# Performance work log

Measured on AMD Instinct MI355X. Metric: run time of the kernel, lower is better.

## Reference

```python
import jax, jax.numpy as jnp
import numpy as np

NUM_HEADS = 16
D_MODEL = 1024
DEPTH = D_MODEL // NUM_HEADS
THRESHOLD = 0.1
BATCH = 2
SEQ = 2048


def setup_inputs() -> dict:
    key = jax.random.key(0)
    ks = jax.random.split(key, 9)
    w_scale = 1.0 / np.sqrt(D_MODEL)
    Q = jax.random.normal(ks[0], (BATCH, SEQ, D_MODEL), dtype=jnp.float32)
    T = jax.random.normal(ks[1], (BATCH, SEQ, D_MODEL), dtype=jnp.float32)
    V = jax.random.normal(ks[2], (BATCH, SEQ, D_MODEL), dtype=jnp.float32)
    Wq = jax.random.normal(ks[3], (NUM_HEADS, D_MODEL, DEPTH), dtype=jnp.float32) * w_scale
    Wk = jax.random.normal(ks[4], (NUM_HEADS, D_MODEL, DEPTH), dtype=jnp.float32) * w_scale
    Wv = jax.random.normal(ks[5], (NUM_HEADS, D_MODEL, DEPTH), dtype=jnp.float32) * w_scale
    Wo = jax.random.normal(ks[6], (D_MODEL, D_MODEL), dtype=jnp.float32) * w_scale
    bq = jnp.zeros((NUM_HEADS, DEPTH), dtype=jnp.float32)
    bk = jnp.zeros((NUM_HEADS, DEPTH), dtype=jnp.float32)
    bv = jnp.zeros((NUM_HEADS, DEPTH), dtype=jnp.float32)
    bo = jnp.zeros((D_MODEL,), dtype=jnp.float32)
    return {"Q": Q, "T": T, "V": V, "Wq": Wq, "bq": bq, "Wk": Wk, "bk": bk,
            "Wv": Wv, "bv": bv, "Wo": Wo, "bo": bo}


def reference(Q, T, V, Wq, bq, Wk, bk, Wv, bv, Wo, bo):
    # Per-head projections (stacked over heads): [B,S,D] x [H,D,E] -> [B,H,S,E]
    q = jnp.einsum('bsd,hde->bhse', Q, Wq) + bq[None, :, None, :]
    k = jnp.einsum('bsd,hde->bhse', T, Wk) + bk[None, :, None, :]
    v = jnp.einsum('bsd,hde->bhse', V, Wv) + bv[None, :, None, :]

    # Raw scores (NOT pre-scaled): [B,H,S,S]
    scores = jnp.einsum('bhqe,bhke->bhqk', q, k)
    # tf.where(A>thr, A, -2**32 * cast(A>thr)) -> failing entries become 0
    scores = jnp.where(scores > THRESHOLD, scores, jnp.zeros((), scores.dtype))
    # M = 1 - lower_band(ones): +1 on strictly upper-triangular entries
    seq = scores.shape[-1]
    upper = jnp.triu(jnp.ones((seq, seq), dtype=scores.dtype), k=1)
    scores = (scores + upper) / jnp.sqrt(jnp.asarray(DEPTH, scores.dtype))

    attn = jax.nn.softmax(scores, axis=-1)
    out = jnp.einsum('bhqk,bhke->bhqe', attn, v)  # [B,H,S,E]
    B, H, S, E = out.shape
    concat = out.transpose(0, 2, 1, 3).reshape(B, S, H * E)  # [B,S,D]
    return concat @ Wo + bo
```

## Files before the change

kernel.cpp:

```cpp
#include <hip/hip_runtime.h>
#include <stdint.h>


typedef __attribute__((ext_vector_type(8))) short bf16x8;
typedef __attribute__((ext_vector_type(4))) float f32x4;

#define DEVFN static __device__ __forceinline__

static constexpr int S_ = 2048;
static constexpr int H_ = 16;

DEVFN unsigned short f2bf(float x) {
  union { float f; uint32_t u; } v; v.f = x;
  const uint32_t r = v.u + 0x7fffu + ((v.u >> 16) & 1u);
  return (unsigned short)(r >> 16);
}

DEVFN f32x4 fzero() { f32x4 v = {0.f, 0.f, 0.f, 0.f}; return v; }

union U8 { uint32_t u[4]; bf16x8 v; };

DEVFN void gld_lds16(const void* g, void* lds) {
  __builtin_amdgcn_global_load_lds(
      (const __attribute__((address_space(1))) void*)g,
      (__attribute__((address_space(3))) void*)lds, 16, 0, 0);
}

__global__ void prep_weights(const float* __restrict__ Wq, const float* __restrict__ Wk,
                             const float* __restrict__ Wv, const float* __restrict__ Wo,
                             unsigned short* __restrict__ dstBase) {
  const int z = blockIdx.z;
  const float* src = (z == 0) ? Wq : (z == 1) ? Wk : (z == 2) ? Wv : Wo;
  unsigned short* dst = dstBase + (size_t)z * (1024u * 1024u);
  const int idx = blockIdx.x * 256 + threadIdx.x;
  const int c = idx & 1023;
  const int d0 = (idx >> 10) << 3;
  unsigned short hv[8];
#pragma unroll
  for (int t = 0; t < 8; ++t) {
    const int d = d0 + t;
    const float v = (z < 3) ? src[(size_t)((c >> 6) * 1024 + d) * 64 + (c & 63)]
                            : src[(size_t)d * 1024 + c];
    hv[t] = f2bf(v);
  }
  *(uint4*)(dst + (size_t)c * 1024 + d0) = *(const uint4*)hv;
}

__global__ __launch_bounds__(256, 3)
void proj_gemm(const float* __restrict__ Qm, const float* __restrict__ Tm,
               const float* __restrict__ Vm, const unsigned short* __restrict__ Wt,
               const float* __restrict__ bq, const float* __restrict__ bk,
               const float* __restrict__ bv, unsigned short* __restrict__ qb,
               unsigned short* __restrict__ kb, unsigned short* __restrict__ vtb) {
  __shared__ float Af[2][128 * 32];
  __shared__ unsigned short Bt[2][128 * 32];

  const int tid = threadIdx.x;
  const int lane = tid & 63;
  const int w = tid >> 6;
  const int g = lane >> 4, c = lane & 15;
  const int wm = w >> 1, wn = w & 1;

  const int orig = blockIdx.x;
  const int xcd = orig & 7;
  const int l = orig >> 3;
  const int bx = xcd * 4 + l / 24;
  const int by = l % 24;

  const int m0 = bx * 128;
  const int proj = by >> 3;
  const int n0 = (by & 7) * 128;

  const float* Asrc = (proj == 0) ? Qm : (proj == 1) ? Tm : Vm;
  const unsigned short* W = Wt + (size_t)proj * (1024u * 1024u);

  f32x4 acc[4][4];
#pragma unroll
  for (int i = 0; i < 4; ++i)
#pragma unroll
    for (int j = 0; j < 4; ++j) acc[i][j] = fzero();

  const int arow = w * 8 + (lane >> 3);
  const int ach = lane & 7;
  const int brow = w * 16 + (lane >> 2);
  const int bch = lane & 3;

  auto stage = [&](int kt, int buf) {
#pragma unroll
    for (int u = 0; u < 4; ++u) {
      const int row = u * 32 + arow;
      const int ch = ach ^ (row & 7);
      gld_lds16(Asrc + (size_t)(m0 + row) * 1024 + kt * 32 + ch * 4,
                &Af[buf][(u * 32 + w * 8) * 32]);
    }
#pragma unroll
    for (int u = 0; u < 2; ++u) {
      const int row = u * 64 + brow;
      const int ch = bch ^ ((row >> 1) & 3);
      gld_lds16(W + (size_t)(n0 + row) * 1024 + kt * 32 + ch * 8,
                &Bt[buf][(u * 64 + w * 16) * 32]);
    }
  };

  stage(0, 0);
  __syncthreads();

  for (int kt = 0; kt < 32; ++kt) {
    const int buf = kt & 1;
    if (kt < 31) stage(kt + 1, buf ^ 1);

    bf16x8 af[4], bfr[4];
#pragma unroll
    for (int mi = 0; mi < 4; ++mi) {
      const int row = wm * 64 + mi * 16 + c;
      const int swz = row & 7;
      const float4 fa = *(const float4*)&Af[buf][row * 32 + ((2 * g) ^ swz) * 4];
      const float4 fb = *(const float4*)&Af[buf][row * 32 + ((2 * g + 1) ^ swz) * 4];
      U8 u8;
      asm("v_cvt_pk_bf16_f32 %0, %1, %2" : "=v"(u8.u[0]) : "v"(fa.x), "v"(fa.y));
      asm("v_cvt_pk_bf16_f32 %0, %1, %2" : "=v"(u8.u[1]) : "v"(fa.z), "v"(fa.w));
      asm("v_cvt_pk_bf16_f32 %0, %1, %2" : "=v"(u8.u[2]) : "v"(fb.x), "v"(fb.y));
      asm("v_cvt_pk_bf16_f32 %0, %1, %2" : "=v"(u8.u[3]) : "v"(fb.z), "v"(fb.w));
      af[mi] = u8.v;
    }
#pragma unroll
    for (int ni = 0; ni < 4; ++ni) {
      const int row = wn * 64 + ni * 16 + c;
      bfr[ni] = *(const bf16x8*)&Bt[buf][row * 32 + ((g ^ ((row >> 1) & 3))) * 8];
    }
#pragma unroll
    for (int mi = 0; mi < 4; ++mi)
#pragma unroll
      for (int ni = 0; ni < 4; ++ni)
        acc[mi][ni] = __builtin_amdgcn_mfma_f32_16x16x32_bf16(af[mi], bfr[ni],
                                                              acc[mi][ni], 0, 0, 0);
    __syncthreads();
  }

  const float* bias = (proj == 0) ? bq : (proj == 1) ? bk : bv;
  if (proj < 2) {
    unsigned short* dptr = (proj == 0) ? qb : kb;
#pragma unroll
    for (int ni = 0; ni < 4; ++ni) {
      const int colb = n0 + wn * 64 + ni * 16 + c;
      const float bc = bias[colb];
      const int hh = colb >> 6, e = colb & 63;
#pragma unroll
      for (int mi = 0; mi < 4; ++mi)
#pragma unroll
        for (int r = 0; r < 4; ++r) {
          const int row = m0 + wm * 64 + mi * 16 + g * 4 + r;
          const int bb = row >> 11, s = row & 2047;
          dptr[(((size_t)(bb * H_ + hh)) * S_ + s) * 64 + e] = f2bf(acc[mi][ni][r] + bc);
        }
    }
  } else {
#pragma unroll
    for (int ni = 0; ni < 4; ++ni) {
      const int colb = n0 + wn * 64 + ni * 16 + c;
      const float bc = bias[colb];
      const int hh = colb >> 6, e = colb & 63;
#pragma unroll
      for (int mi = 0; mi < 4; ++mi) {
        const int rowb = m0 + wm * 64 + mi * 16 + g * 4;
        const int bb = rowb >> 11, s0 = rowb & 2047;
        const float v0 = acc[mi][ni][0] + bc, v1 = acc[mi][ni][1] + bc;
        const float v2 = acc[mi][ni][2] + bc, v3 = acc[mi][ni][3] + bc;
        uint2 pk;
        asm("v_cvt_pk_bf16_f32 %0, %1, %2" : "=v"(pk.x) : "v"(v0), "v"(v1));
        asm("v_cvt_pk_bf16_f32 %0, %1, %2" : "=v"(pk.y) : "v"(v2), "v"(v3));
        *(uint2*)&vtb[(((size_t)(bb * H_ + hh)) * 64 + e) * S_ + s0] = pk;
      }
    }
  }
}

__global__ __launch_bounds__(256, 2)
void attn_kernel(const unsigned short* __restrict__ qb,
                 const unsigned short* __restrict__ kb,
                 const unsigned short* __restrict__ vtb,
                 unsigned short* __restrict__ att) {
  __shared__ unsigned short Kt[2][64 * 64];
  __shared__ unsigned short Vt[2][64 * 64];
  __shared__ unsigned short Pt[4][32 * 64];

  const int tid = threadIdx.x;
  const int lane = tid & 63;
  const int w = tid >> 6;
  const int g = lane >> 4, c = lane & 15;

  const int orig = blockIdx.x;
  const int logical = ((orig & 7) << 6) | (orig >> 3);
  const int qblk = logical & 15;
  const int bh = logical >> 4;
  const int hh = bh & 15, bz = bh >> 4;

  const int q0w = qblk * 128 + w * 32;
  const unsigned short* qh = qb + (size_t)bh * S_ * 64;
  const unsigned short* kh = kb + (size_t)bh * S_ * 64;
  const unsigned short* vh = vtb + (size_t)bh * 64 * S_;

  bf16x8 aq[2][2];
#pragma unroll
  for (int m = 0; m < 2; ++m)
#pragma unroll
    for (int t = 0; t < 2; ++t)
      aq[m][t] = *(const bf16x8*)&qh[(size_t)(q0w + m * 16 + c) * 64 + t * 32 + g * 8];

  bf16x8 onesB;
#pragma unroll
  for (int i = 0; i < 8; ++i) onesB[i] = (short)0x3F80;

  f32x4 O[2][4];
  f32x4 accL[2];
#pragma unroll
  for (int m = 0; m < 2; ++m) {
#pragma unroll
    for (int ne = 0; ne < 4; ++ne) O[m][ne] = fzero();
    accL[m] = fzero();
  }

  constexpr float L2E = 1.4426950408889634f;
  const float S2 = 0.125f * L2E;
  const float B2 = 0.125f * L2E;

  int kvOff[2][4], paOff[2][2], pwOff[2][4];
#pragma unroll
  for (int ks = 0; ks < 2; ++ks) {
#pragma unroll
    for (int mi = 0; mi < 4; ++mi) {
      const int row = mi * 16 + c;
      kvOff[ks][mi] = 2 * (row * 64 + ((ks * 4 + g) ^ (row & 7)) * 8);
    }
#pragma unroll
    for (int m = 0; m < 2; ++m)
      paOff[m][ks] = 2 * ((m * 16 + c) * 64 + ((ks * 4 + g) ^ (c & 7)) * 8);
  }
#pragma unroll
  for (int m = 0; m < 2; ++m)
#pragma unroll
    for (int mi = 0; mi < 4; ++mi)
      pwOff[m][mi] =
          2 * ((m * 16 + c) * 64 + ((2 * mi + (g >> 1)) ^ (c & 7)) * 8 + (g & 1) * 4);

  const int srow = w * 8 + (lane >> 3);
  const int sch = (lane & 7) ^ (srow & 7);
  const unsigned short* kS0 = kh + (size_t)srow * 64 + sch * 8;
  const unsigned short* kS1 = kh + (size_t)(32 + srow) * 64 + sch * 8;
  const unsigned short* vS0 = vh + (size_t)srow * S_ + sch * 8;
  const unsigned short* vS1 = vh + (size_t)(32 + srow) * S_ + sch * 8;

  {
    gld_lds16(kS0, &Kt[0][(w * 8) * 64]);
    gld_lds16(kS1, &Kt[0][(32 + w * 8) * 64]);
    gld_lds16(vS0, &Vt[0][(w * 8) * 64]);
    gld_lds16(vS1, &Vt[0][(32 + w * 8) * 64]);
  }
  __syncthreads();

#define ATTN_BODY(JT, CUR)                                                     \
  do {                                                                         \
    const int j0 = (JT) * 64;                                                  \
    if ((JT) < 31) {                                                           \
      gld_lds16(kS0 + 4096, &Kt[CUR ^ 1][(w * 8) * 64]);                       \
      gld_lds16(kS1 + 4096, &Kt[CUR ^ 1][(32 + w * 8) * 64]);                  \
      gld_lds16(vS0 + 64, &Vt[CUR ^ 1][(w * 8) * 64]);                         \
      gld_lds16(vS1 + 64, &Vt[CUR ^ 1][(32 + w * 8) * 64]);                    \
      kS0 += 4096; kS1 += 4096; vS0 += 64; vS1 += 64;                          \
    }                                                                          \
    f32x4 sa[2][4];                                                            \
    _Pragma("unroll")                                                          \
    for (int m = 0; m < 2; ++m)                                                \
      _Pragma("unroll")                                                        \
      for (int mi = 0; mi < 4; ++mi) sa[m][mi] = fzero();                      \
    __builtin_amdgcn_s_setprio(1);                                             \
    _Pragma("unroll")                                                          \
    for (int ks = 0; ks < 2; ++ks)                                             \
      _Pragma("unroll")                                                        \
      for (int mi = 0; mi < 4; ++mi) {                                         \
        const bf16x8 ka =                                                      \
            *(const bf16x8*)((const char*)&Kt[CUR][0] + kvOff[ks][mi]);        \
        sa[0][mi] = __builtin_amdgcn_mfma_f32_16x16x32_bf16(ka, aq[0][ks],     \
                                                            sa[0][mi], 0, 0, 0);\
        sa[1][mi] = __builtin_amdgcn_mfma_f32_16x16x32_bf16(ka, aq[1][ks],     \
                                                            sa[1][mi], 0, 0, 0);\
      }                                                                        \
    __builtin_amdgcn_s_setprio(0);                                             \
    const bool allUp = (j0 >= q0w + 32);                                       \
    const bool noneUp = (j0 + 63 <= q0w);                                      \
    _Pragma("unroll")                                                          \
    for (int m = 0; m < 2; ++m) {                                              \
      const int iq = q0w + m * 16 + c;                                         \
      _Pragma("unroll")                                                        \
      for (int mi = 0; mi < 4; ++mi) {                                         \
        float pv[4];                                                           \
        if (allUp || noneUp) {                                                 \
          const float bb = allUp ? B2 : 0.f;                                   \
          _Pragma("unroll")                                                    \
          for (int r = 0; r < 4; ++r) {                                        \
            const float v = sa[m][mi][r];                                      \
            pv[r] = __builtin_amdgcn_exp2f(                                    \
                (v > 0.1f) ? __builtin_fmaf(v, S2, bb) : bb);                  \
          }                                                                    \
        } else {                                                               \
          _Pragma("unroll")                                                    \
          for (int r = 0; r < 4; ++r) {                                        \
            const float v = sa[m][mi][r];                                      \
            const float bb = (j0 + mi * 16 + g * 4 + r > iq) ? B2 : 0.f;       \
            pv[r] = __builtin_amdgcn_exp2f(                                    \
                (v > 0.1f) ? __builtin_fmaf(v, S2, bb) : bb);                  \
          }                                                                    \
        }                                                                      \
        uint2 d;                                                               \
        asm("v_cvt_pk_bf16_f32 %0, %1, %2"                                     \
            : "=v"(d.x) : "v"(pv[0]), "v"(pv[1]));                             \
        asm("v_cvt_pk_bf16_f32 %0, %1, %2"                                     \
            : "=v"(d.y) : "v"(pv[2]), "v"(pv[3]));                             \
        *(uint2*)((char*)&Pt[w][0] + pwOff[m][mi]) = d;                        \
      }                                                                        \
    }                                                                          \
    asm volatile("s_waitcnt lgkmcnt(0)" ::: "memory");                         \
    __builtin_amdgcn_sched_barrier(0);                                         \
    __builtin_amdgcn_s_setprio(1);                                             \
    _Pragma("unroll")                                                          \
    for (int ks = 0; ks < 2; ++ks) {                                           \
      const bf16x8 pa0 =                                                       \
          *(const bf16x8*)((const char*)&Pt[w][0] + paOff[0][ks]);             \
      const bf16x8 pa1 =                                                       \
          *(const bf16x8*)((const char*)&Pt[w][0] + paOff[1][ks]);             \
      accL[0] = __builtin_amdgcn_mfma_f32_16x16x32_bf16(pa0, onesB, accL[0],   \
                                                        0, 0, 0);              \
      accL[1] = __builtin_amdgcn_mfma_f32_16x16x32_bf16(pa1, onesB, accL[1],   \
                                                        0, 0, 0);              \
      _Pragma("unroll")                                                        \
      for (int ne = 0; ne < 4; ++ne) {                                         \
        const bf16x8 bv8 =                                                     \
            *(const bf16x8*)((const char*)&Vt[CUR][0] + kvOff[ks][ne]);        \
        O[0][ne] = __builtin_amdgcn_mfma_f32_16x16x32_bf16(pa0, bv8, O[0][ne], \
                                                           0, 0, 0);           \
        O[1][ne] = __builtin_amdgcn_mfma_f32_16x16x32_bf16(pa1, bv8, O[1][ne], \
                                                           0, 0, 0);           \
      }                                                                        \
    }                                                                          \
    __builtin_amdgcn_s_setprio(0);                                             \
    __syncthreads();                                                           \
  } while (0)

  for (int jt = 0; jt < 32; jt += 2) {
    ATTN_BODY(jt, 0);
    ATTN_BODY(jt + 1, 1);
  }
#undef ATTN_BODY

#pragma unroll
  for (int m = 0; m < 2; ++m)
#pragma unroll
    for (int r = 0; r < 4; ++r) {
      const float il = 1.f / accL[m][r];
      const int qg = q0w + m * 16 + g * 4 + r;
      const size_t ro = ((size_t)(bz * S_ + qg)) * 1024 + hh * 64;
#pragma unroll
      for (int ne = 0; ne < 4; ++ne)
        att[ro + ne * 16 + c] = f2bf(O[m][ne][r] * il);
    }
}

__global__ __launch_bounds__(256, 3)
void out_gemm(const unsigned short* __restrict__ att,
              const unsigned short* __restrict__ WoT,
              const float* __restrict__ bo, float* __restrict__ outp) {
  __shared__ unsigned short At[2][128 * 32];
  __shared__ unsigned short Bt[2][128 * 32];

  const int tid = threadIdx.x;
  const int lane = tid & 63;
  const int w = tid >> 6;
  const int g = lane >> 4, c = lane & 15;
  const int wm = w >> 1, wn = w & 1;

  const int orig = blockIdx.x;
  const int xcd = orig & 7;
  const int l = orig >> 3;
  const int bx = xcd * 4 + l / 8;
  const int by = l % 8;
  const int m0 = bx * 128;
  const int n0 = by * 128;

  f32x4 acc[4][4];
#pragma unroll
  for (int i = 0; i < 4; ++i)
#pragma unroll
    for (int j = 0; j < 4; ++j) acc[i][j] = fzero();

  const int srow = lane >> 2;
  const int sch = lane & 3;

  auto stage = [&](int kt, int buf) {
#pragma unroll
    for (int u = 0; u < 2; ++u) {
      const int row = u * 64 + w * 16 + srow;
      const int ch = sch ^ ((row >> 1) & 3);
      gld_lds16(att + (size_t)(m0 + row) * 1024 + kt * 32 + ch * 8,
                &At[buf][(u * 64 + w * 16) * 32]);
      gld_lds16(WoT + (size_t)(n0 + row) * 1024 + kt * 32 + ch * 8,
                &Bt[buf][(u * 64 + w * 16) * 32]);
    }
  };

  stage(0, 0);
  __syncthreads();

  for (int kt = 0; kt < 32; ++kt) {
    const int buf = kt & 1;
    if (kt < 31) stage(kt + 1, buf ^ 1);

    bf16x8 af[4], bfr[4];
#pragma unroll
    for (int mi = 0; mi < 4; ++mi) {
      const int row = wm * 64 + mi * 16 + c;
      af[mi] = *(const bf16x8*)&At[buf][row * 32 + ((g ^ ((row >> 1) & 3))) * 8];
    }
#pragma unroll
    for (int ni = 0; ni < 4; ++ni) {
      const int row = wn * 64 + ni * 16 + c;
      bfr[ni] = *(const bf16x8*)&Bt[buf][row * 32 + ((g ^ ((row >> 1) & 3))) * 8];
    }
#pragma unroll
    for (int mi = 0; mi < 4; ++mi)
#pragma unroll
      for (int ni = 0; ni < 4; ++ni)
        acc[mi][ni] = __builtin_amdgcn_mfma_f32_16x16x32_bf16(af[mi], bfr[ni],
                                                              acc[mi][ni], 0, 0, 0);
    __syncthreads();
  }

#pragma unroll
  for (int ni = 0; ni < 4; ++ni) {
    const int colb = n0 + wn * 64 + ni * 16 + c;
    const float bc = bo[colb];
#pragma unroll
    for (int mi = 0; mi < 4; ++mi)
#pragma unroll
      for (int r = 0; r < 4; ++r) {
        const int row = m0 + wm * 64 + mi * 16 + g * 4 + r;
        outp[(size_t)row * 1024 + colb] = acc[mi][ni][r] + bc;
      }
  }
}

extern "C" void kernel_launch(void* const* d_in, const int* in_sizes, int n_in,
                              void* d_out, int out_size, void* d_ws, size_t ws_size,
                              hipStream_t stream) {
  const float* Q  = (const float*)d_in[0];
  const float* T  = (const float*)d_in[1];
  const float* V  = (const float*)d_in[2];
  const float* Wq = (const float*)d_in[3];
  const float* bq = (const float*)d_in[4];
  const float* Wk = (const float*)d_in[5];
  const float* bk = (const float*)d_in[6];
  const float* Wv = (const float*)d_in[7];
  const float* bv = (const float*)d_in[8];
  const float* Wo = (const float*)d_in[9];
  const float* bo = (const float*)d_in[10];

  const size_t MB = 1024ull * 1024ull;
  if (ws_size < 40 * MB) return;

  uint8_t* ws = (uint8_t*)d_ws;
  unsigned short* Wt  = (unsigned short*)(ws);
  unsigned short* qb  = (unsigned short*)(ws + 8 * MB);
  unsigned short* kb  = (unsigned short*)(ws + 16 * MB);
  unsigned short* vtb = (unsigned short*)(ws + 24 * MB);
  unsigned short* attb = (unsigned short*)(ws + 32 * MB);

  prep_weights<<<dim3(512, 1, 4), 256, 0, stream>>>(Wq, Wk, Wv, Wo, Wt);
  proj_gemm<<<dim3(768), 256, 0, stream>>>(Q, T, V, Wt, bq, bk, bv,
                                           qb, kb, vtb);
  attn_kernel<<<dim3(512), 256, 0, stream>>>(qb, kb, vtb, attb);
  out_gemm<<<dim3(256), 256, 0, stream>>>(attb, Wt + 3ull * 1024ull * 1024ull,
                                          bo, (float*)d_out);
}
```

Baseline: 132.0 us.

## Stage 128-key K/V tiles per barrier in attention kernel

Doubles the K/V LDS staging tile from 64 to 128 keys per iteration, processing two 64-key sub-blocks between each __syncthreads. The V tile gets a new 128-wide XOR swizzle layout with matching load addresses. This halves the number of block barriers and issues larger prefetch batches. In exchange, LDS use rises to about 80KB per block, which may limit occupancy below the two blocks per CU requested by the launch bounds.

New measurement: 131.5 us (median of 2 runs). No clear change (-0.3%).

```diff
diff --git a/kernel.cpp b/kernel.cpp
--- a/kernel.cpp
+++ b/kernel.cpp
@@ -180,8 +180,8 @@
                  const unsigned short* __restrict__ kb,
                  const unsigned short* __restrict__ vtb,
                  unsigned short* __restrict__ att) {
-  __shared__ unsigned short Kt[2][64 * 64];
-  __shared__ unsigned short Vt[2][64 * 64];
+  __shared__ unsigned short Kt[2][128 * 64];
+  __shared__ unsigned short Vt[2][64 * 128];
   __shared__ unsigned short Pt[4][32 * 64];
 
   const int tid = threadIdx.x;
@@ -224,18 +224,29 @@
   const float S2 = 0.125f * L2E;
   const float B2 = 0.125f * L2E;
 
-  int kvOff[2][4], paOff[2][2], pwOff[2][4];
+  int kaOff[2][4];
+  int vOff[2][2][4];
+  int paOff[2][2], pwOff[2][4];
 #pragma unroll
   for (int ks = 0; ks < 2; ++ks) {
 #pragma unroll
     for (int mi = 0; mi < 4; ++mi) {
       const int row = mi * 16 + c;
-      kvOff[ks][mi] = 2 * (row * 64 + ((ks * 4 + g) ^ (row & 7)) * 8);
+      kaOff[ks][mi] = 2 * (row * 64 + ((ks * 4 + g) ^ (row & 7)) * 8);
     }
 #pragma unroll
     for (int m = 0; m < 2; ++m)
       paOff[m][ks] = 2 * ((m * 16 + c) * 64 + ((ks * 4 + g) ^ (c & 7)) * 8);
   }
+#pragma unroll
+  for (int s = 0; s < 2; ++s)
+#pragma unroll
+    for (int ks = 0; ks < 2; ++ks)
+#pragma unroll
+      for (int ne = 0; ne < 4; ++ne) {
+        const int e = ne * 16 + c;
+        vOff[s][ks][ne] = 2 * (e * 128 + ((s * 8 + ks * 4 + g) ^ c) * 8);
+      }
 #pragma unroll
   for (int m = 0; m < 2; ++m)
 #pragma unroll
@@ -243,31 +254,25 @@
       pwOff[m][mi] =
           2 * ((m * 16 + c) * 64 + ((2 * mi + (g >> 1)) ^ (c & 7)) * 8 + (g & 1) * 4);
 
-  const int srow = w * 8 + (lane >> 3);
-  const int sch = (lane & 7) ^ (srow & 7);
-  const unsigned short* kS0 = kh + (size_t)srow * 64 + sch * 8;
-  const unsigned short* kS1 = kh + (size_t)(32 + srow) * 64 + sch * 8;
-  const unsigned short* vS0 = vh + (size_t)srow * S_ + sch * 8;
-  const unsigned short* vS1 = vh + (size_t)(32 + srow) * S_ + sch * 8;
+  const int srowK = w * 8 + (lane >> 3);
+  const int schK = (lane & 7) ^ (srowK & 7);
+  const unsigned short* kS = kh + (size_t)srowK * 64 + schK * 8;
+  const int rowV = w * 4 + (lane >> 4);
+  const int jV = (lane & 15) ^ rowV;
+  const unsigned short* vS = vh + (size_t)rowV * S_ + jV * 8;
 
   {
-    gld_lds16(kS0, &Kt[0][(w * 8) * 64]);
-    gld_lds16(kS1, &Kt[0][(32 + w * 8) * 64]);
-    gld_lds16(vS0, &Vt[0][(w * 8) * 64]);
-    gld_lds16(vS1, &Vt[0][(32 + w * 8) * 64]);
+#pragma unroll
+    for (int u = 0; u < 4; ++u) {
+      gld_lds16(kS + u * 2048, &Kt[0][(u * 32 + w * 8) * 64]);
+      gld_lds16(vS + (size_t)u * 32768, &Vt[0][(u * 16 + w * 4) * 128]);
+    }
   }
   __syncthreads();
 
-#define ATTN_BODY(JT, CUR)                                                     \
+#define ATTN_SUB(J0S, SB, CUR)                                                 \
   do {                                                                         \
-    const int j0 = (JT) * 64;                                                  \
-    if ((JT) < 31) {                                                           \
-      gld_lds16(kS0 + 4096, &Kt[CUR ^ 1][(w * 8) * 64]);                       \
-      gld_lds16(kS1 + 4096, &Kt[CUR ^ 1][(32 + w * 8) * 64]);                  \
-      gld_lds16(vS0 + 64, &Vt[CUR ^ 1][(w * 8) * 64]);                         \
-      gld_lds16(vS1 + 64, &Vt[CUR ^ 1][(32 + w * 8) * 64]);                    \
-      kS0 += 4096; kS1 += 4096; vS0 += 64; vS1 += 64;                          \
-    }                                                                          \
+    const int j0 = (J0S);                                                      \
     f32x4 sa[2][4];                                                            \
     _Pragma("unroll")                                                          \
     for (int m = 0; m < 2; ++m)                                                \
@@ -278,8 +283,8 @@
     for (int ks = 0; ks < 2; ++ks)                                             \
       _Pragma("unroll")                                                        \
       for (int mi = 0; mi < 4; ++mi) {                                         \
-        const bf16x8 ka =                                                      \
-            *(const bf16x8*)((const char*)&Kt[CUR][0] + kvOff[ks][mi]);        \
+        const bf16x8 ka = *(const bf16x8*)((const char*)&Kt[CUR][0] +          \
+                                           (SB) * 8192 + kaOff[ks][mi]);       \
         sa[0][mi] = __builtin_amdgcn_mfma_f32_16x16x32_bf16(ka, aq[0][ks],     \
                                                             sa[0][mi], 0, 0, 0);\
         sa[1][mi] = __builtin_amdgcn_mfma_f32_16x16x32_bf16(ka, aq[1][ks],     \
@@ -334,8 +339,8 @@
                                                         0, 0, 0);              \
       _Pragma("unroll")                                                        \
       for (int ne = 0; ne < 4; ++ne) {                                         \
-        const bf16x8 bv8 =                                                     \
-            *(const bf16x8*)((const char*)&Vt[CUR][0] + kvOff[ks][ne]);        \
+        const bf16x8 bv8 = *(const bf16x8*)((const char*)&Vt[CUR][0] +         \
+                                            vOff[SB][ks][ne]);                 \
         O[0][ne] = __builtin_amdgcn_mfma_f32_16x16x32_bf16(pa0, bv8, O[0][ne], \
                                                            0, 0, 0);           \
         O[1][ne] = __builtin_amdgcn_mfma_f32_16x16x32_bf16(pa1, bv8, O[1][ne], \
@@ -343,14 +348,30 @@
       }                                                                        \
     }                                                                          \
     __builtin_amdgcn_s_setprio(0);                                             \
-    __syncthreads();                                                           \
   } while (0)
 
-  for (int jt = 0; jt < 32; jt += 2) {
-    ATTN_BODY(jt, 0);
-    ATTN_BODY(jt + 1, 1);
-  }
-#undef ATTN_BODY
+#define ATTN_TILE(T, CUR)                                                      \
+  do {                                                                         \
+    if ((T) < 15) {       \
+      _Pragma("unroll")                                                        \
+      for (int u = 0; u < 4; ++u) {                                            \
+        gld_lds16(kS + 8192 + u * 2048, &Kt[CUR ^ 1][(u * 32 + w * 8) * 64]);  \
+        gld_lds16(vS + 128 + (size_t)u * 32768,                                \
+                  &Vt[CUR ^ 1][(u * 16 + w * 4) * 128]);                       \
+      }                                                                        \
+      kS += 8192; vS += 128;                                                   \
+    }                                                                          \
+    ATTN_SUB((T) * 128, 0, CUR);                                               \
+    ATTN_SUB((T) * 128 + 64, 1, CUR);                                          \
+    __syncthreads();         \
+  } while (0)
+
+  for (int T = 0; T < 16; T += 2) {
+    ATTN_TILE(T, 0);
+    ATTN_TILE(T + 1, 1);
+  }
+#undef ATTN_TILE
+#undef ATTN_SUB
 
 #pragma unroll
   for (int m = 0; m < 2; ++m)
```
